# Kernel tuning notes

Measured on AMD Instinct MI355X. Metric: run time of the kernel, lower is better.

Reference implementation:

```python
import jax, jax.numpy as jnp
import numpy as np

E = 200000      # n_edges
IN = 128        # input_nf
HID = 32        # hidden_nf
H = 4           # att_heads
OUT = 128       # output_nf
MAXK = 16       # MAX_K neighbor slots


def setup_inputs() -> dict:
    key = jax.random.key(0)
    ks = jax.random.split(key, 12)
    Z = jax.random.normal(ks[0], (E, IN), dtype=jnp.float32)
    idx = jax.random.randint(ks[1], (E, 2, MAXK), 0, E)
    red = jax.random.uniform(ks[2], (E, 1, MAXK)) < 0.15
    klist = jnp.where(red, -1, idx).astype(jnp.int64)
    s = 0.05  # xavier-ish scale
    Wq = jax.random.normal(ks[3], (H, HID, IN), dtype=jnp.float32) * s
    Wk = jax.random.normal(ks[4], (H, HID, IN), dtype=jnp.float32) * s
    Wv = jax.random.normal(ks[5], (H, HID, IN), dtype=jnp.float32) * s
    Wb = jax.random.normal(ks[6], (H, 1, IN), dtype=jnp.float32) * s
    Wg = jax.random.normal(ks[7], (H, HID, IN), dtype=jnp.float32) * s
    bg = jnp.zeros((H, HID), dtype=jnp.float32)
    Wout = jax.random.normal(ks[8], (OUT, H * HID), dtype=jnp.float32) * s
    bout = jnp.zeros((OUT,), dtype=jnp.float32)
    return {"Z": Z, "klist": klist, "Wq": Wq, "Wk": Wk, "Wv": Wv,
            "Wb": Wb, "Wg": Wg, "bg": bg, "Wout": Wout, "bout": bout}


def reference(Z, klist, Wq, Wk, Wv, Wb, Wg, bg, Wout, bout):
    idx_i, idx_j = klist[:, 0], klist[:, 1]          # (E, K)
    red = idx_i == -1
    valid = (~red).astype(Z.dtype)[..., None]        # (E, K, 1)
    ii = jnp.where(red, 0, idx_i)
    jj = jnp.where(red, 0, idx_j)
    scale = 1.0 / np.sqrt(HID)
    outs = []
    for h in range(H):  # att_heads: small fixed loop over structurally distinct heads
        q = Z @ Wq[h].T                              # (E, HID)
        k = Z @ Wk[h].T
        v = Z @ Wv[h].T
        b = (Z @ Wb[h].T)[:, 0]                      # (E,)
        g = jax.nn.sigmoid(Z @ Wg[h].T + bg[h])      # (E, HID)
        tri_k = jnp.take(k, ii, axis=0) * valid      # (E, K, HID), redundant slots zeroed
        tri_v = jnp.take(v, ii, axis=0) * valid
        tri_b = jnp.take(b, jj, axis=0) * valid[..., 0]  # (E, K)
        scores = scale * jnp.einsum('eh,ekh->ek', q, tri_k) + tri_b
        alpha = jax.nn.softmax(scores, axis=1)       # (E, K)
        att = jnp.einsum('ek,ekh->eh', alpha, tri_v) # (E, HID)
        outs.append(g * att)
    out = jnp.concatenate(outs, axis=-1) @ Wout.T + bout  # (E, OUT)
    # dropout is identity in eval mode
    return out
```

## Files before the change

### kernel.cpp

```cpp
#include <hip/hip_runtime.h>
#include <hip/hip_bf16.h>
#include <stdint.h>

#define EDGES 200000
#define INF   128
#define HID   32
#define NHEAD 4
#define OUTF  128
#define MAXK  16

#define NPAD  528
#define NTILES 33

typedef unsigned short u16;
typedef __attribute__((ext_vector_type(8))) short bf16x8;
typedef __attribute__((ext_vector_type(4))) float f32x4;

__device__ __forceinline__ u16 f2bf(float f) {
  union { float f; uint32_t u; } v; v.f = f;
  uint32_t u = v.u;
  return (u16)((u + 0x7FFFu + ((u >> 16) & 1u)) >> 16);
}
__device__ __forceinline__ float bflo(uint32_t p) {
  union { uint32_t u; float f; } v; v.u = p << 16;
  return v.f;
}
__device__ __forceinline__ float bfhi(uint32_t p) {
  union { uint32_t u; float f; } v; v.u = p & 0xFFFF0000u;
  return v.f;
}

__device__ __forceinline__ uint32_t cvtpk_bf16(float lo, float hi) {
  float2 t; t.x = lo; t.y = hi;
  __hip_bfloat162 h = __float22bfloat162_rn(t);
  uint32_t u;
  __builtin_memcpy(&u, &h, 4);
  return u;
}
__device__ __forceinline__ bf16x8 pack8(float4 f0, float4 f1) {
  union { uint32_t u[4]; bf16x8 v; } r;
  r.u[0] = cvtpk_bf16(f0.x, f0.y);
  r.u[1] = cvtpk_bf16(f0.z, f0.w);
  r.u[2] = cvtpk_bf16(f1.x, f1.y);
  r.u[3] = cvtpk_bf16(f1.z, f1.w);
  return r.v;
}
__device__ __forceinline__ float sigm(float x) {
  return 1.0f / (1.0f + __expf(-x));
}

template <int CTRL>
__device__ __forceinline__ float dpp_add(float x) {
  int y = __builtin_amdgcn_update_dpp(0, __builtin_bit_cast(int, x),
                                      CTRL, 0xF, 0xF, true);
  return x + __builtin_bit_cast(float, y);
}
__device__ __forceinline__ float row16_sum(float x) {
  x = dpp_add<0xB1>(x);
  x = dpp_add<0x4E>(x);
  x = dpp_add<0x141>(x);
  x = dpp_add<0x140>(x);
  return x;
}

struct AccPair { f32x4 a, b; };
__device__ __forceinline__ AccPair tile_mm(const u16* __restrict__ W, int row0,
                                           int ml, int blk,
                                           const bf16x8 (&zfr)[2][4], int ldw) {
  bf16x8 wfr[4];
#pragma unroll
  for (int kk = 0; kk < 4; ++kk)
    wfr[kk] = *(const bf16x8*)(W + (size_t)(row0 + ml) * ldw + kk * 32 + blk * 8);
  AccPair r;
  r.a = (f32x4){0.f, 0.f, 0.f, 0.f};
  r.b = (f32x4){0.f, 0.f, 0.f, 0.f};
#pragma unroll
  for (int kk = 0; kk < 4; ++kk) {
    r.a = __builtin_amdgcn_mfma_f32_16x16x32_bf16(wfr[kk], zfr[0][kk], r.a, 0, 0, 0);
    r.b = __builtin_amdgcn_mfma_f32_16x16x32_bf16(wfr[kk], zfr[1][kk], r.b, 0, 0, 0);
  }
  return r;
}

__global__ __launch_bounds__(256) void prep_kernel(
    const float* __restrict__ Wq, const float* __restrict__ Wk,
    const float* __restrict__ Wv, const float* __restrict__ Wb,
    const float* __restrict__ Wg, const float* __restrict__ Wout,
    u16* __restrict__ Wc, u16* __restrict__ Woutb)
{
  int t = blockIdx.x * 256 + threadIdx.x;
  if (t < NPAD * INF) {
    int n = t >> 7, k = t & 127;
    float v = 0.0f;
    if (n < 128)       v = Wq[n * 128 + k];
    else if (n < 256)  v = Wg[(n - 128) * 128 + k];
    else if (n < 512) {
      int m = n - 256, h = m >> 6, c = m & 63;
      v = (c < 32) ? Wk[(h * 32 + c) * 128 + k] : Wv[(h * 32 + (c - 32)) * 128 + k];
    } else if (n < 516) v = Wb[(n - 512) * 128 + k];
    Wc[t] = f2bf(v);
  } else if (t < NPAD * INF + OUTF * 128) {
    int u = t - NPAD * INF;
    Woutb[u] = f2bf(Wout[u]);
  }
}

__global__ __launch_bounds__(256) void proj_kernel(
    const float* __restrict__ Z, const u16* __restrict__ Wc,
    const float* __restrict__ bg,
    u16* __restrict__ qb, u16* __restrict__ gb,
    u16* __restrict__ kvb, float* __restrict__ bb)
{
  const int wid = threadIdx.x >> 6, lane = threadIdx.x & 63;
  const int ml = lane & 15, blk = lane >> 4;
  const long e0 = (long)blockIdx.x * 128 + wid * 32;
  if (e0 >= EDGES) return;

  bf16x8 zfr[2][4];
#pragma unroll
  for (int s = 0; s < 2; ++s) {
    const float* zp = Z + (e0 + s * 16 + ml) * INF + blk * 8;
#pragma unroll
    for (int kk = 0; kk < 4; ++kk) {
      float4 f0 = *(const float4*)(zp + kk * 32);
      float4 f1 = *(const float4*)(zp + kk * 32 + 4);
      zfr[s][kk] = pack8(f0, f1);
    }
  }

  const long eA = e0 + ml, eB = e0 + 16 + ml;

  for (int nt = 0; nt < 8; ++nt) {
    AccPair acc = tile_mm(Wc, nt * 16, ml, blk, zfr, INF);
    const int n0 = nt * 16 + blk * 4;
    uint2 pa, pb;
    pa.x = cvtpk_bf16(acc.a[0], acc.a[1]); pa.y = cvtpk_bf16(acc.a[2], acc.a[3]);
    pb.x = cvtpk_bf16(acc.b[0], acc.b[1]); pb.y = cvtpk_bf16(acc.b[2], acc.b[3]);
    *(uint2*)(qb + eA * 128 + n0) = pa;
    *(uint2*)(qb + eB * 128 + n0) = pb;
  }

  for (int nt = 8; nt < 16; ++nt) {
    AccPair acc = tile_mm(Wc, nt * 16, ml, blk, zfr, INF);
    const int ng = (nt - 8) * 16 + blk * 4;
    float4 b4 = *(const float4*)(bg + ng);
    float a0 = sigm(acc.a[0] + b4.x), a1 = sigm(acc.a[1] + b4.y);
    float a2 = sigm(acc.a[2] + b4.z), a3 = sigm(acc.a[3] + b4.w);
    float c0 = sigm(acc.b[0] + b4.x), c1 = sigm(acc.b[1] + b4.y);
    float c2 = sigm(acc.b[2] + b4.z), c3 = sigm(acc.b[3] + b4.w);
    uint2 pa, pb;
    pa.x = cvtpk_bf16(a0, a1); pa.y = cvtpk_bf16(a2, a3);
    pb.x = cvtpk_bf16(c0, c1); pb.y = cvtpk_bf16(c2, c3);
    *(uint2*)(gb + eA * 128 + ng) = pa;
    *(uint2*)(gb + eB * 128 + ng) = pb;
  }

  for (int nt = 16; nt < 32; ++nt) {
    AccPair acc = tile_mm(Wc, nt * 16, ml, blk, zfr, INF);
    const int nk = (nt - 16) * 16 + blk * 4;
    uint2 pa, pb;
    pa.x = cvtpk_bf16(acc.a[0], acc.a[1]); pa.y = cvtpk_bf16(acc.a[2], acc.a[3]);
    pb.x = cvtpk_bf16(acc.b[0], acc.b[1]); pb.y = cvtpk_bf16(acc.b[2], acc.b[3]);
    *(uint2*)(kvb + eA * 256 + nk) = pa;
    *(uint2*)(kvb + eB * 256 + nk) = pb;
  }

  {
    AccPair acc = tile_mm(Wc, 512, ml, blk, zfr, INF);
    if (blk == 0) {
      *(float4*)(bb + eA * 4) = make_float4(acc.a[0], acc.a[1], acc.a[2], acc.a[3]);
      *(float4*)(bb + eB * 4) = make_float4(acc.b[0], acc.b[1], acc.b[2], acc.b[3]);
    }
  }
}

__global__ __launch_bounds__(256) void attn_kernel(
    const int* __restrict__ klist, const u16* qb,
    const u16* __restrict__ gb, const u16* __restrict__ kvb,
    const float* __restrict__ bb, u16* xb)
{
  const int wid = threadIdx.x >> 6;
  const int lane = threadIdx.x & 63;
  int e = blockIdx.x * 4 + wid;
  e = __builtin_amdgcn_readfirstlane(e);
  if (e >= EDGES) return;

  const int h = lane >> 4;
  const uint32_t q2 = *(const uint32_t*)(qb + (size_t)e * 128 + 2 * lane);
  const uint32_t g2 = *(const uint32_t*)(gb + (size_t)e * 128 + 2 * lane);
  const float q0 = bflo(q2), q1 = bfhi(q2);
  const int kvo = h * 64 + (lane & 15) * 2;
  const float scale = 0.17677669529663687f;

  float sc[MAXK];
  uint32_t vvm[MAXK];
  const int* kl = klist + (size_t)e * 32;
#pragma unroll
  for (int nb = 0; nb < MAXK; ++nb) {
    const int ii = kl[nb];
    const int jj = kl[16 + nb];
    const bool valid = (ii >= 0);
    const int is = valid ? ii : 0;
    const int js = valid ? jj : 0;
    const u16* kvrow = kvb + (size_t)is * 256;
    uint32_t kki = *(const uint32_t*)(kvrow + kvo);
    uint32_t vvi = *(const uint32_t*)(kvrow + kvo + 32);
    float p = q0 * bflo(kki) + q1 * bfhi(kki);
    p = row16_sum(p);
    float bj = bb[(size_t)js * 4 + h];
    sc[nb]  = valid ? (scale * p + bj) : 0.0f;
    vvm[nb] = valid ? vvi : 0u;
  }

  float m = sc[0];
#pragma unroll
  for (int nb = 1; nb < MAXK; ++nb) m = fmaxf(m, sc[nb]);
  float s = 0.f, a0 = 0.f, a1 = 0.f;
#pragma unroll
  for (int nb = 0; nb < MAXK; ++nb) {
    float al = __expf(sc[nb] - m);
    s += al;
    a0 += al * bflo(vvm[nb]);
    a1 += al * bfhi(vvm[nb]);
  }
  float inv = 1.0f / s;
  u16 x0 = f2bf(bflo(g2) * a0 * inv);
  u16 x1 = f2bf(bfhi(g2) * a1 * inv);
  uint32_t xo = (uint32_t)x0 | ((uint32_t)x1 << 16);
  *(uint32_t*)(xb + (size_t)e * 128 + 2 * lane) = xo;
}

__global__ __launch_bounds__(256) void outgemm_kernel(
    const u16* xb, const u16* __restrict__ Woutb,
    const float* __restrict__ bout, float* __restrict__ out)
{
  const int wid = threadIdx.x >> 6, lane = threadIdx.x & 63;
  const int ml = lane & 15, blk = lane >> 4;
  const long e0 = (long)blockIdx.x * 128 + wid * 32;
  if (e0 >= EDGES) return;

  bf16x8 xfr[2][4];
#pragma unroll
  for (int s = 0; s < 2; ++s) {
    const u16* xp = xb + (e0 + s * 16 + ml) * 128 + blk * 8;
#pragma unroll
    for (int kk = 0; kk < 4; ++kk)
      xfr[s][kk] = *(const bf16x8*)(xp + kk * 32);
  }

  const long eA = e0 + ml, eB = e0 + 16 + ml;

#pragma unroll
  for (int nt = 0; nt < 8; ++nt) {
    AccPair acc = tile_mm(Woutb, nt * 16, ml, blk, xfr, 128);
    const int o0 = nt * 16 + blk * 4;
    float4 b4 = *(const float4*)(bout + o0);
    float4 ra = make_float4(acc.a[0] + b4.x, acc.a[1] + b4.y,
                            acc.a[2] + b4.z, acc.a[3] + b4.w);
    float4 rb = make_float4(acc.b[0] + b4.x, acc.b[1] + b4.y,
                            acc.b[2] + b4.z, acc.b[3] + b4.w);
    *(float4*)(out + eA * 128 + o0) = ra;
    *(float4*)(out + eB * 128 + o0) = rb;
  }
}

extern "C" void kernel_launch(void* const* d_in, const int* in_sizes, int n_in,
                              void* d_out, int out_size, void* d_ws, size_t ws_size,
                              hipStream_t stream) {
  const float* Z     = (const float*)d_in[0];
  const int*   klist = (const int*)  d_in[1];
  const float* Wq    = (const float*)d_in[2];
  const float* Wk    = (const float*)d_in[3];
  const float* Wv    = (const float*)d_in[4];
  const float* Wb    = (const float*)d_in[5];
  const float* Wg    = (const float*)d_in[6];
  const float* bg    = (const float*)d_in[7];
  const float* Wout  = (const float*)d_in[8];
  const float* bout  = (const float*)d_in[9];
  float* out = (float*)d_out;

  char* ws = (char*)d_ws;
  u16*   Wc    = (u16*)(ws);
  u16*   Woutb = (u16*)(ws + 135168);
  u16*   qb    = (u16*)(ws + 167936);
  u16*   gb    = (u16*)(ws + 51367936);
  u16*   kvb   = (u16*)(ws + 102567936);
  float* bb    = (float*)(ws + 204967936);
  u16*   xb    = qb;

  prep_kernel<<<(NPAD * INF + OUTF * 128 + 255) / 256, 256, 0, stream>>>(
      Wq, Wk, Wv, Wb, Wg, Wout, Wc, Woutb);
  proj_kernel<<<(EDGES + 127) / 128, 256, 0, stream>>>(
      Z, Wc, bg, qb, gb, kvb, bb);
  attn_kernel<<<(EDGES + 3) / 4, 256, 0, stream>>>(
      klist, qb, gb, kvb, bb, xb);
  outgemm_kernel<<<(EDGES + 127) / 128, 256, 0, stream>>>(
      xb, Woutb, bout, out);
}
```

Measured before the change: 611.9 us.

## Fuse attention and output projection into one kernel via LDS staging

Merges the attention kernel and the output GEMM kernel. Each 256-thread block handles 32 edges: each wave runs attention for 8 edges in turn and writes the bf16 results into padded shared memory, then all waves run MFMA output tiles over 2 of the 8 column tiles each. This removes the global write and read-back of the intermediate x buffer and one kernel launch. In exchange, each wave now processes edges serially, with a block barrier between the two phases, which may reduce latency hiding for the gather-heavy attention part.

```diff
diff --git a/kernel.cpp b/kernel.cpp
--- a/kernel.cpp
+++ b/kernel.cpp
@@ -11,6 +11,8 @@
 
 #define NPAD  528
 #define NTILES 33
+
+#define XPAD  136
 
 typedef unsigned short u16;
 typedef __attribute__((ext_vector_type(8))) short bf16x8;
@@ -174,84 +176,85 @@
   }
 }
 
-__global__ __launch_bounds__(256) void attn_kernel(
-    const int* __restrict__ klist, const u16* qb,
+__global__ __launch_bounds__(256) void attn_out_kernel(
+    const int* __restrict__ klist, const u16* __restrict__ qb,
     const u16* __restrict__ gb, const u16* __restrict__ kvb,
-    const float* __restrict__ bb, u16* xb)
+    const float* __restrict__ bb, const u16* __restrict__ Woutb,
+    const float* __restrict__ bout, float* __restrict__ out)
 {
+  __shared__ u16 xs[32 * XPAD];
+
   const int wid = threadIdx.x >> 6;
   const int lane = threadIdx.x & 63;
-  int e = blockIdx.x * 4 + wid;
-  e = __builtin_amdgcn_readfirstlane(e);
-  if (e >= EDGES) return;
+  const long e0 = (long)blockIdx.x * 32;
 
   const int h = lane >> 4;
-  const uint32_t q2 = *(const uint32_t*)(qb + (size_t)e * 128 + 2 * lane);
-  const uint32_t g2 = *(const uint32_t*)(gb + (size_t)e * 128 + 2 * lane);
-  const float q0 = bflo(q2), q1 = bfhi(q2);
   const int kvo = h * 64 + (lane & 15) * 2;
   const float scale = 0.17677669529663687f;
 
-  float sc[MAXK];
-  uint32_t vvm[MAXK];
-  const int* kl = klist + (size_t)e * 32;
-#pragma unroll
-  for (int nb = 0; nb < MAXK; ++nb) {
-    const int ii = kl[nb];
-    const int jj = kl[16 + nb];
-    const bool valid = (ii >= 0);
-    const int is = valid ? ii : 0;
-    const int js = valid ? jj : 0;
-    const u16* kvrow = kvb + (size_t)is * 256;
-    uint32_t kki = *(const uint32_t*)(kvrow + kvo);
-    uint32_t vvi = *(const uint32_t*)(kvrow + kvo + 32);
-    float p = q0 * bflo(kki) + q1 * bfhi(kki);
-    p = row16_sum(p);
-    float bj = bb[(size_t)js * 4 + h];
-    sc[nb]  = valid ? (scale * p + bj) : 0.0f;
-    vvm[nb] = valid ? vvi : 0u;
-  }
-
-  float m = sc[0];
-#pragma unroll
-  for (int nb = 1; nb < MAXK; ++nb) m = fmaxf(m, sc[nb]);
-  float s = 0.f, a0 = 0.f, a1 = 0.f;
-#pragma unroll
-  for (int nb = 0; nb < MAXK; ++nb) {
-    float al = __expf(sc[nb] - m);
-    s += al;
-    a0 += al * bflo(vvm[nb]);
-    a1 += al * bfhi(vvm[nb]);
-  }
-  float inv = 1.0f / s;
-  u16 x0 = f2bf(bflo(g2) * a0 * inv);
-  u16 x1 = f2bf(bfhi(g2) * a1 * inv);
-  uint32_t xo = (uint32_t)x0 | ((uint32_t)x1 << 16);
-  *(uint32_t*)(xb + (size_t)e * 128 + 2 * lane) = xo;
-}
-
-__global__ __launch_bounds__(256) void outgemm_kernel(
-    const u16* xb, const u16* __restrict__ Woutb,
-    const float* __restrict__ bout, float* __restrict__ out)
-{
-  const int wid = threadIdx.x >> 6, lane = threadIdx.x & 63;
+#pragma unroll 1
+  for (int it = 0; it < 8; ++it) {
+    const int le = wid * 8 + it;
+    int e = (int)e0 + le;
+    e = __builtin_amdgcn_readfirstlane(e);
+
+    const uint32_t q2 = *(const uint32_t*)(qb + (size_t)e * 128 + 2 * lane);
+    const uint32_t g2 = *(const uint32_t*)(gb + (size_t)e * 128 + 2 * lane);
+    const float q0 = bflo(q2), q1 = bfhi(q2);
+
+    float sc[MAXK];
+    uint32_t vvm[MAXK];
+    const int* kl = klist + (size_t)e * 32;
+#pragma unroll
+    for (int nb = 0; nb < MAXK; ++nb) {
+      const int ii = kl[nb];
+      const int jj = kl[16 + nb];
+      const bool valid = (ii >= 0);
+      const int is = valid ? ii : 0;
+      const int js = valid ? jj : 0;
+      const u16* kvrow = kvb + (size_t)is * 256;
+      uint32_t kki = *(const uint32_t*)(kvrow + kvo);
+      uint32_t vvi = *(const uint32_t*)(kvrow + kvo + 32);
+      float p = q0 * bflo(kki) + q1 * bfhi(kki);
+      p = row16_sum(p);
+      float bj = bb[(size_t)js * 4 + h];
+      sc[nb]  = valid ? (scale * p + bj) : 0.0f;
+      vvm[nb] = valid ? vvi : 0u;
+    }
+
+    float m = sc[0];
+#pragma unroll
+    for (int nb = 1; nb < MAXK; ++nb) m = fmaxf(m, sc[nb]);
+    float s = 0.f, a0 = 0.f, a1 = 0.f;
+#pragma unroll
+    for (int nb = 0; nb < MAXK; ++nb) {
+      float al = __expf(sc[nb] - m);
+      s += al;
+      a0 += al * bflo(vvm[nb]);
+      a1 += al * bfhi(vvm[nb]);
+    }
+    float inv = 1.0f / s;
+    uint32_t xo = cvtpk_bf16(bflo(g2) * a0 * inv, bfhi(g2) * a1 * inv);
+    *(uint32_t*)(&xs[le * XPAD + 2 * lane]) = xo;
+  }
+
+  __syncthreads();
+
   const int ml = lane & 15, blk = lane >> 4;
-  const long e0 = (long)blockIdx.x * 128 + wid * 32;
-  if (e0 >= EDGES) return;
 
   bf16x8 xfr[2][4];
 #pragma unroll
   for (int s = 0; s < 2; ++s) {
-    const u16* xp = xb + (e0 + s * 16 + ml) * 128 + blk * 8;
 #pragma unroll
     for (int kk = 0; kk < 4; ++kk)
-      xfr[s][kk] = *(const bf16x8*)(xp + kk * 32);
+      xfr[s][kk] = *(const bf16x8*)(&xs[(s * 16 + ml) * XPAD + kk * 32 + blk * 8]);
   }
 
   const long eA = e0 + ml, eB = e0 + 16 + ml;
 
 #pragma unroll
-  for (int nt = 0; nt < 8; ++nt) {
+  for (int t = 0; t < 2; ++t) {
+    const int nt = wid * 2 + t;
     AccPair acc = tile_mm(Woutb, nt * 16, ml, blk, xfr, 128);
     const int o0 = nt * 16 + blk * 4;
     float4 b4 = *(const float4*)(bout + o0);
@@ -286,14 +289,11 @@
   u16*   gb    = (u16*)(ws + 51367936);
   u16*   kvb   = (u16*)(ws + 102567936);
   float* bb    = (float*)(ws + 204967936);
-  u16*   xb    = qb;
 
   prep_kernel<<<(NPAD * INF + OUTF * 128 + 255) / 256, 256, 0, stream>>>(
       Wq, Wk, Wv, Wb, Wg, Wout, Wc, Woutb);
   proj_kernel<<<(EDGES + 127) / 128, 256, 0, stream>>>(
       Z, Wc, bg, qb, gb, kvb, bb);
-  attn_kernel<<<(EDGES + 3) / 4, 256, 0, stream>>>(
-      klist, qb, gb, kvb, bb, xb);
-  outgemm_kernel<<<(EDGES + 127) / 128, 256, 0, stream>>>(
-      xb, Woutb, bout, out);
-}
+  attn_out_kernel<<<EDGES / 32, 256, 0, stream>>>(
+      klist, qb, gb, kvb, bb, Woutb, bout, out);
+}
```

Result: faster. 563.4 us (-7.9%).
